# Kernel optimization log

Hardware: AMD Instinct MI355X
Metric: run time of the kernel (lower is better)

The kernel has to match this reference:

```python
import jax, jax.numpy as jnp
import numpy as np

MAX_DISPLACEMENT = 4


def setup_inputs() -> dict:
    key = jax.random.key(0)
    k1, k2 = jax.random.split(key)
    B, C, H, W = 8, 128, 128, 256
    features1 = jax.random.normal(k1, (B, C, H, W), dtype=jnp.float32)
    features2 = jax.random.normal(k2, (B, C, H, W), dtype=jnp.float32)
    return {"features1": features1, "features2": features2}


def _cost_volume(features1, features2, max_displacement):
    B, C, H, W = features1.shape
    d = max_displacement
    # zero-pad features2 spatially by d (uflow compute_cost_volume semantics)
    padded = jnp.pad(features2, ((0, 0), (0, 0), (d, d), (d, d)))
    num_shifts = 2 * d + 1
    costs = []
    for i in range(num_shifts):          # fixed small structural loop: (2d+1)^2 = 81
        for j in range(num_shifts):
            shifted = jax.lax.dynamic_slice(padded, (0, 0, i, j), (B, C, H, W))
            # mean over channel dim of elementwise product
            costs.append(jnp.mean(features1 * shifted, axis=1))
    return jnp.stack(costs, axis=1)  # [B, (2d+1)^2, H, W]


def reference(features1, features2):
    return _cost_volume(features1, features2, MAX_DISPLACEMENT)
```

## Files before the change

kernel.cpp:

```cpp
#include <hip/hip_runtime.h>

#define B_  8
#define C_  128
#define H_  128
#define W_  256
#define HW_ (H_ * W_)
#define TH  8
#define TW  32
#define NPAIR 4
#define F2RS 72
#define F2PT (16 * F2RS)
#define F1RS 36
#define F1PT (8 * F1RS)
#define F1OFF (NPAIR * F2PT)
#define BUFN (F1OFF + NPAIR * F1PT)
#define NTHREADS 576

typedef __fp16 h2 __attribute__((ext_vector_type(2)));

__device__ __forceinline__ float dot2f16(unsigned int a, unsigned int b, float c) {
#if __has_builtin(__builtin_amdgcn_fdot2)
    return __builtin_amdgcn_fdot2(__builtin_bit_cast(h2, a),
                                  __builtin_bit_cast(h2, b), c, false);
#else
    h2 ha = __builtin_bit_cast(h2, a), hb = __builtin_bit_cast(h2, b);
    return c + (float)ha.x * (float)hb.x + (float)ha.y * (float)hb.y;
#endif
}

__device__ __forceinline__ unsigned int pk(float x, float y) {
    h2 r = __builtin_amdgcn_cvt_pkrtz(x, y);
    return __builtin_bit_cast(unsigned int, r);
}

__global__ __launch_bounds__(NTHREADS, 3) void cv_kernel(
    const float* __restrict__ f1g, const float* __restrict__ f2g,
    float* __restrict__ outg) {
    __shared__ __align__(16) unsigned int lds[2][BUFN];

    const int tid = threadIdx.x;
    const int w0 = blockIdx.x * TW;
    const int h0 = blockIdx.y * TH;
    const int b  = blockIdx.z;

    const bool roleA = (tid < 512);
    int offA = 0, ldA = 0;
    float mA = 0.f;
    if (roleA) {
        int pp = tid >> 7, r = (tid >> 3) & 15, u = tid & 7;
        int gh = h0 - 4 + r, gw = w0 - 4 + 4 * u;
        bool valid = (gh >= 0) && (gh < H_) && (gw >= 0) && (gw <= W_ - 4);
        int ghc = min(max(gh, 0), H_ - 1);
        int gwc = min(max(gw, 0), W_ - 4);
        offA = ((b * C_ + 2 * pp) * H_ + ghc) * W_ + gwc;
        ldA  = pp * F2PT + r * F2RS + 4 * u;
        mA   = valid ? 1.f : 0.f;
    }
    const bool roleC = (tid < 384);
    int offC = 0, ldC = 0;
    float mC = 0.f;
    const float* pC = f1g;
    if (tid < 128) {
        int pp = tid >> 5, r = (tid >> 1) & 15, u = 8 + (tid & 1);
        int gh = h0 - 4 + r, gw = w0 - 4 + 4 * u;
        bool valid = (gh >= 0) && (gh < H_) && (gw >= 0) && (gw <= W_ - 4);
        int ghc = min(max(gh, 0), H_ - 1);
        int gwc = min(max(gw, 0), W_ - 4);
        offC = ((b * C_ + 2 * pp) * H_ + ghc) * W_ + gwc;
        pC   = f2g;
        ldC  = pp * F2PT + r * F2RS + 4 * u;
        mC   = valid ? 1.f : 0.f;
    } else if (tid < 384) {
        int t = tid - 128;
        int pp = t >> 6, r = (t >> 3) & 7, u = t & 7;
        offC = ((b * C_ + 2 * pp) * H_ + h0 + r) * W_ + w0 + 4 * u;
        pC   = f1g;
        ldC  = F1OFF + pp * F1PT + r * F1RS + 4 * u;
        mC   = 1.f;
    }

#define LOADST()                                                              \
    do {                                                                      \
        if (roleA) {                                                          \
            aA = *(const float4*)(f2g + offA);                                \
            bA = *(const float4*)(f2g + offA + HW_);                          \
            offA += 8 * HW_;                                                  \
        }                                                                     \
        if (roleC) {                                                          \
            cC = *(const float4*)(pC + offC);                                 \
            dC = *(const float4*)(pC + offC + HW_);                           \
            offC += 8 * HW_;                                                  \
        }                                                                     \
    } while (0)

#define STOREST(bi)                                                           \
    do {                                                                      \
        if (roleA) {                                                          \
            uint4 wv;                                                         \
            wv.x = pk(aA.x * mA, bA.x * mA);                                  \
            wv.y = pk(aA.y * mA, bA.y * mA);                                  \
            wv.z = pk(aA.z * mA, bA.z * mA);                                  \
            wv.w = pk(aA.w * mA, bA.w * mA);                                  \
            *(uint4*)(&lds[bi][ldA]) = wv;                                    \
        }                                                                     \
        if (roleC) {                                                          \
            uint4 w2;                                                         \
            w2.x = pk(cC.x * mC, dC.x * mC);                                  \
            w2.y = pk(cC.y * mC, dC.y * mC);                                  \
            w2.z = pk(cC.z * mC, dC.z * mC);                                  \
            w2.w = pk(cC.w * mC, dC.w * mC);                                  \
            *(uint4*)(&lds[bi][ldC]) = w2;                                    \
        }                                                                     \
    } while (0)

#define BAR()                                                                 \
    do {                                                                      \
        asm volatile("s_waitcnt lgkmcnt(0)" ::: "memory");                    \
        __builtin_amdgcn_s_barrier();                                         \
    } while (0)

    const int di   = tid >> 6;
    const int lane = tid & 63;
    const int hh   = lane >> 3;
    const int sc   = lane & 7;
    const int rd0  = (hh + di) * F2RS + 4 * sc;
    const int rf0  = F1OFF + hh * F1RS + 4 * sc;

    float acc[9][4];
#pragma unroll
    for (int j = 0; j < 9; ++j)
#pragma unroll
        for (int p = 0; p < 4; ++p) acc[j][p] = 0.f;

#define COMPUTE(bi)                                                           \
    do {                                                                      \
        _Pragma("unroll 2")                                                   \
        for (int q = 0; q < NPAIR; ++q) {                                     \
            const unsigned int* bf2 = &lds[bi][q * F2PT];                     \
            const unsigned int* bf1 = &lds[bi][q * F1PT];                     \
            uint4 fa = *(const uint4*)(bf2 + rd0);                            \
            uint4 fb = *(const uint4*)(bf2 + rd0 + 4);                        \
            uint4 fc = *(const uint4*)(bf2 + rd0 + 8);                        \
            uint4 ga = *(const uint4*)(bf1 + rf0);                            \
            unsigned int f2u[12] = {fa.x, fa.y, fa.z, fa.w, fb.x, fb.y,       \
                                    fb.z, fb.w, fc.x, fc.y, fc.z, fc.w};      \
            unsigned int f1u[4]  = {ga.x, ga.y, ga.z, ga.w};                  \
            _Pragma("unroll")                                                 \
            for (int j = 0; j < 9; ++j)                                       \
                _Pragma("unroll")                                             \
                for (int p = 0; p < 4; ++p)                                   \
                    acc[j][p] = dot2f16(f1u[p], f2u[p + j], acc[j][p]);       \
        }                                                                     \
    } while (0)

    float4 aA, bA, cC, dC;

    LOADST();
    STOREST(0);
    BAR();

    for (int st = 0; st < 14; st += 2) {
        LOADST();
        COMPUTE(0);
        STOREST(1);
        BAR();
        LOADST();
        COMPUTE(1);
        STOREST(0);
        BAR();
    }
    LOADST();
    COMPUTE(0);
    STOREST(1);
    BAR();
    COMPUTE(1);

    const float inv = 1.0f / 128.0f;
    int obase = ((b * 81 + di * 9) * H_ + h0 + hh) * W_ + w0 + 4 * sc;
#pragma unroll
    for (int j = 0; j < 9; ++j) {
        float4 o = make_float4(acc[j][0] * inv, acc[j][1] * inv,
                               acc[j][2] * inv, acc[j][3] * inv);
        *(float4*)(outg + obase) = o;
        obase += HW_;
    }
}

extern "C" void kernel_launch(void* const* d_in, const int* in_sizes, int n_in,
                              void* d_out, int out_size, void* d_ws, size_t ws_size,
                              hipStream_t stream) {
    const float* f1 = (const float*)d_in[0];
    const float* f2 = (const float*)d_in[1];
    float* out = (float*)d_out;
    dim3 grid(W_ / TW, H_ / TH, B_);
    cv_kernel<<<grid, NTHREADS, 0, stream>>>(f1, f2, out);
}
```

Baseline: 124.3 us.

## Split displacement rows across three blocks with smaller 192-thread blocks

```diff
diff --git a/kernel.cpp b/kernel.cpp
--- a/kernel.cpp
+++ b/kernel.cpp
@@ -7,14 +7,14 @@
 #define HW_ (H_ * W_)
 #define TH  8
 #define TW  32
-#define NPAIR 4
-#define F2RS 72
-#define F2PT (16 * F2RS)
-#define F1RS 36
-#define F1PT (8 * F1RS)
-#define F1OFF (NPAIR * F2PT)
-#define BUFN (F1OFF + NPAIR * F1PT)
-#define NTHREADS 576
+#define F2R   10
+#define F2RS  48
+#define F2PT  (F2R * F2RS)
+#define F1RS  40
+#define F1PT  (TH * F1RS)
+#define F1OFF (2 * F2PT)
+#define BUFN  (F1OFF + 2 * F1PT)
+#define NTHREADS 192
 
 typedef __fp16 h2 __attribute__((ext_vector_type(2)));
 
@@ -41,75 +41,74 @@
     const int tid = threadIdx.x;
     const int w0 = blockIdx.x * TW;
     const int h0 = blockIdx.y * TH;
-    const int b  = blockIdx.z;
+    const int g  = blockIdx.z % 3;
+    const int b  = blockIdx.z / 3;
+    const int dib = 3 * g;
 
-    const bool roleA = (tid < 512);
-    int offA = 0, ldA = 0;
-    float mA = 0.f;
-    if (roleA) {
-        int pp = tid >> 7, r = (tid >> 3) & 15, u = tid & 7;
-        int gh = h0 - 4 + r, gw = w0 - 4 + 4 * u;
+    int offA, ldA;
+    float mA;
+    {
+        int p  = (tid >= 100);
+        int ul = tid - p * 100;
+        int r  = ul / 10, u = ul - 10 * r;
+        int gh = h0 - 4 + dib + r, gw = w0 - 4 + 4 * u;
         bool valid = (gh >= 0) && (gh < H_) && (gw >= 0) && (gw <= W_ - 4);
         int ghc = min(max(gh, 0), H_ - 1);
         int gwc = min(max(gw, 0), W_ - 4);
-        offA = ((b * C_ + 2 * pp) * H_ + ghc) * W_ + gwc;
-        ldA  = pp * F2PT + r * F2RS + 4 * u;
+        offA = ((b * C_ + 2 * p) * H_ + ghc) * W_ + gwc;
+        ldA  = p * F2PT + r * F2RS + 4 * u;
         mA   = valid ? 1.f : 0.f;
     }
-    const bool roleC = (tid < 384);
+    const bool roleC = (tid < 136);
     int offC = 0, ldC = 0;
     float mC = 0.f;
     const float* pC = f1g;
-    if (tid < 128) {
-        int pp = tid >> 5, r = (tid >> 1) & 15, u = 8 + (tid & 1);
-        int gh = h0 - 4 + r, gw = w0 - 4 + 4 * u;
+    if (tid < 8) {
+        int r = 9, u = 2 + tid;
+        int gh = h0 - 4 + dib + r, gw = w0 - 4 + 4 * u;
         bool valid = (gh >= 0) && (gh < H_) && (gw >= 0) && (gw <= W_ - 4);
         int ghc = min(max(gh, 0), H_ - 1);
         int gwc = min(max(gw, 0), W_ - 4);
-        offC = ((b * C_ + 2 * pp) * H_ + ghc) * W_ + gwc;
+        offC = ((b * C_ + 2) * H_ + ghc) * W_ + gwc;
         pC   = f2g;
-        ldC  = pp * F2PT + r * F2RS + 4 * u;
+        ldC  = F2PT + r * F2RS + 4 * u;
         mC   = valid ? 1.f : 0.f;
-    } else if (tid < 384) {
-        int t = tid - 128;
-        int pp = t >> 6, r = (t >> 3) & 7, u = t & 7;
-        offC = ((b * C_ + 2 * pp) * H_ + h0 + r) * W_ + w0 + 4 * u;
+    } else if (roleC) {
+        int t = tid - 8;
+        int p = t >> 6, r = (t >> 3) & 7, u = t & 7;
+        offC = ((b * C_ + 2 * p) * H_ + h0 + r) * W_ + w0 + 4 * u;
         pC   = f1g;
-        ldC  = F1OFF + pp * F1PT + r * F1RS + 4 * u;
+        ldC  = F1OFF + p * F1PT + r * F1RS + 4 * u;
         mC   = 1.f;
     }
 
 #define LOADST()                                                              \
     do {                                                                      \
-        if (roleA) {                                                          \
-            aA = *(const float4*)(f2g + offA);                                \
-            bA = *(const float4*)(f2g + offA + HW_);                          \
-            offA += 8 * HW_;                                                  \
-        }                                                                     \
+        aA = *(const float4*)(f2g + offA);                                    \
+        bA = *(const float4*)(f2g + offA + HW_);                              \
+        offA += 4 * HW_;                                                      \
         if (roleC) {                                                          \
             cC = *(const float4*)(pC + offC);                                 \
             dC = *(const float4*)(pC + offC + HW_);                           \
-            offC += 8 * HW_;                                                  \
+            offC += 4 * HW_;                                                  \
         }                                                                     \
     } while (0)
 
 #define STOREST(bi)                                                           \
     do {                                                                      \
-        if (roleA) {                                                          \
-            uint4 wv;                                                         \
-            wv.x = pk(aA.x * mA, bA.x * mA);                                  \
-            wv.y = pk(aA.y * mA, bA.y * mA);                                  \
-            wv.z = pk(aA.z * mA, bA.z * mA);                                  \
-            wv.w = pk(aA.w * mA, bA.w * mA);                                  \
-            *(uint4*)(&lds[bi][ldA]) = wv;                                    \
-        }                                                                     \
+        uint4 wv_;                                                            \
+        wv_.x = pk(aA.x * mA, bA.x * mA);                                     \
+        wv_.y = pk(aA.y * mA, bA.y * mA);                                     \
+        wv_.z = pk(aA.z * mA, bA.z * mA);                                     \
+        wv_.w = pk(aA.w * mA, bA.w * mA);                                     \
+        *(uint4*)(&lds[bi][ldA]) = wv_;                                       \
         if (roleC) {                                                          \
-            uint4 w2;                                                         \
-            w2.x = pk(cC.x * mC, dC.x * mC);                                  \
-            w2.y = pk(cC.y * mC, dC.y * mC);                                  \
-            w2.z = pk(cC.z * mC, dC.z * mC);                                  \
-            w2.w = pk(cC.w * mC, dC.w * mC);                                  \
-            *(uint4*)(&lds[bi][ldC]) = w2;                                    \
+            uint4 w2_;                                                        \
+            w2_.x = pk(cC.x * mC, dC.x * mC);                                 \
+            w2_.y = pk(cC.y * mC, dC.y * mC);                                 \
+            w2_.z = pk(cC.z * mC, dC.z * mC);                                 \
+            w2_.w = pk(cC.w * mC, dC.w * mC);                                 \
+            *(uint4*)(&lds[bi][ldC]) = w2_;                                   \
         }                                                                     \
     } while (0)
 
@@ -119,11 +118,11 @@
         __builtin_amdgcn_s_barrier();                                         \
     } while (0)
 
-    const int di   = tid >> 6;
+    const int wv   = tid >> 6;
     const int lane = tid & 63;
     const int hh   = lane >> 3;
     const int sc   = lane & 7;
-    const int rd0  = (hh + di) * F2RS + 4 * sc;
+    const int rd0  = (hh + wv) * F2RS + 4 * sc;
     const int rf0  = F1OFF + hh * F1RS + 4 * sc;
 
     float acc[9][4];
@@ -134,8 +133,8 @@
 
 #define COMPUTE(bi)                                                           \
     do {                                                                      \
-        _Pragma("unroll 2")                                                   \
-        for (int q = 0; q < NPAIR; ++q) {                                     \
+        _Pragma("unroll")                                                     \
+        for (int q = 0; q < 2; ++q) {                                         \
             const unsigned int* bf2 = &lds[bi][q * F2PT];                     \
             const unsigned int* bf1 = &lds[bi][q * F1PT];                     \
             uint4 fa = *(const uint4*)(bf2 + rd0);                            \
@@ -159,7 +158,7 @@
     STOREST(0);
     BAR();
 
-    for (int st = 0; st < 14; st += 2) {
+    for (int st = 0; st < 30; st += 2) {
         LOADST();
         COMPUTE(0);
         STOREST(1);
@@ -176,6 +175,7 @@
     COMPUTE(1);
 
     const float inv = 1.0f / 128.0f;
+    const int di = dib + wv;
     int obase = ((b * 81 + di * 9) * H_ + h0 + hh) * W_ + w0 + 4 * sc;
 #pragma unroll
     for (int j = 0; j < 9; ++j) {
@@ -192,6 +192,6 @@
     const float* f1 = (const float*)d_in[0];
     const float* f2 = (const float*)d_in[1];
     float* out = (float*)d_out;
-    dim3 grid(W_ / TW, H_ / TH, B_);
+    dim3 grid(W_ / TW, H_ / TH, B_ * 3);
     cv_kernel<<<grid, NTHREADS, 0, stream>>>(f1, f2, out);
 }
```

After: 152.7 us. +22.8%, slower.

## Deepen global-load prefetch to two stages and pad f1 LDS row stride

Applied to the files above, without the earlier changes.

```diff
diff --git a/kernel.cpp b/kernel.cpp
--- a/kernel.cpp
+++ b/kernel.cpp
@@ -10,7 +10,7 @@
 #define NPAIR 4
 #define F2RS 72
 #define F2PT (16 * F2RS)
-#define F1RS 36
+#define F1RS 40
 #define F1PT (8 * F1RS)
 #define F1OFF (NPAIR * F2PT)
 #define BUFN (F1OFF + NPAIR * F1PT)
@@ -79,36 +79,36 @@
         mC   = 1.f;
     }
 
-#define LOADST()                                                              \
+#define LOADST(Sa, Sb, Sc, Sd)                                                \
     do {                                                                      \
         if (roleA) {                                                          \
-            aA = *(const float4*)(f2g + offA);                                \
-            bA = *(const float4*)(f2g + offA + HW_);                          \
+            Sa = *(const float4*)(f2g + offA);                                \
+            Sb = *(const float4*)(f2g + offA + HW_);                          \
             offA += 8 * HW_;                                                  \
         }                                                                     \
         if (roleC) {                                                          \
-            cC = *(const float4*)(pC + offC);                                 \
-            dC = *(const float4*)(pC + offC + HW_);                           \
+            Sc = *(const float4*)(pC + offC);                                 \
+            Sd = *(const float4*)(pC + offC + HW_);                           \
             offC += 8 * HW_;                                                  \
         }                                                                     \
     } while (0)
 
-#define STOREST(bi)                                                           \
+#define STOREST(bi, Sa, Sb, Sc, Sd)                                           \
     do {                                                                      \
         if (roleA) {                                                          \
             uint4 wv;                                                         \
-            wv.x = pk(aA.x * mA, bA.x * mA);                                  \
-            wv.y = pk(aA.y * mA, bA.y * mA);                                  \
-            wv.z = pk(aA.z * mA, bA.z * mA);                                  \
-            wv.w = pk(aA.w * mA, bA.w * mA);                                  \
+            wv.x = pk(Sa.x * mA, Sb.x * mA);                                  \
+            wv.y = pk(Sa.y * mA, Sb.y * mA);                                  \
+            wv.z = pk(Sa.z * mA, Sb.z * mA);                                  \
+            wv.w = pk(Sa.w * mA, Sb.w * mA);                                  \
             *(uint4*)(&lds[bi][ldA]) = wv;                                    \
         }                                                                     \
         if (roleC) {                                                          \
             uint4 w2;                                                         \
-            w2.x = pk(cC.x * mC, dC.x * mC);                                  \
-            w2.y = pk(cC.y * mC, dC.y * mC);                                  \
-            w2.z = pk(cC.z * mC, dC.z * mC);                                  \
-            w2.w = pk(cC.w * mC, dC.w * mC);                                  \
+            w2.x = pk(Sc.x * mC, Sd.x * mC);                                  \
+            w2.y = pk(Sc.y * mC, Sd.y * mC);                                  \
+            w2.z = pk(Sc.z * mC, Sd.z * mC);                                  \
+            w2.w = pk(Sc.w * mC, Sd.w * mC);                                  \
             *(uint4*)(&lds[bi][ldC]) = w2;                                    \
         }                                                                     \
     } while (0)
@@ -153,25 +153,25 @@
         }                                                                     \
     } while (0)
 
-    float4 aA, bA, cC, dC;
+    float4 aA, bA, cA, dA, aB, bB, cB, dB;
 
-    LOADST();
-    STOREST(0);
+    LOADST(aA, bA, cA, dA);
+    LOADST(aB, bB, cB, dB);
+    STOREST(0, aA, bA, cA, dA);
     BAR();
 
-    for (int st = 0; st < 14; st += 2) {
-        LOADST();
+    for (int s = 0; s < 14; s += 2) {
+        LOADST(aA, bA, cA, dA);
         COMPUTE(0);
-        STOREST(1);
+        STOREST(1, aB, bB, cB, dB);
         BAR();
-        LOADST();
+        LOADST(aB, bB, cB, dB);
         COMPUTE(1);
-        STOREST(0);
+        STOREST(0, aA, bA, cA, dA);
         BAR();
     }
-    LOADST();
     COMPUTE(0);
-    STOREST(1);
+    STOREST(1, aB, bB, cB, dB);
     BAR();
     COMPUTE(1);
 
```

New measurement: 130.7 us. 5.2% more time.

## Drop ninth wavefront by splitting last displacement row across two waves

Applied to the files above, without the earlier changes.

```diff
diff --git a/kernel.cpp b/kernel.cpp
--- a/kernel.cpp
+++ b/kernel.cpp
@@ -10,11 +10,11 @@
 #define NPAIR 4
 #define F2RS 72
 #define F2PT (16 * F2RS)
-#define F1RS 36
+#define F1RS 40
 #define F1PT (8 * F1RS)
 #define F1OFF (NPAIR * F2PT)
 #define BUFN (F1OFF + NPAIR * F1PT)
-#define NTHREADS 576
+#define NTHREADS 512
 
 typedef __fp16 h2 __attribute__((ext_vector_type(2)));
 
@@ -33,7 +33,7 @@
     return __builtin_bit_cast(unsigned int, r);
 }
 
-__global__ __launch_bounds__(NTHREADS, 3) void cv_kernel(
+__global__ __launch_bounds__(NTHREADS, 4) void cv_kernel(
     const float* __restrict__ f1g, const float* __restrict__ f2g,
     float* __restrict__ outg) {
     __shared__ __align__(16) unsigned int lds[2][BUFN];
@@ -43,10 +43,9 @@
     const int h0 = blockIdx.y * TH;
     const int b  = blockIdx.z;
 
-    const bool roleA = (tid < 512);
-    int offA = 0, ldA = 0;
-    float mA = 0.f;
-    if (roleA) {
+    int offA, ldA;
+    float mA;
+    {
         int pp = tid >> 7, r = (tid >> 3) & 15, u = tid & 7;
         int gh = h0 - 4 + r, gw = w0 - 4 + 4 * u;
         bool valid = (gh >= 0) && (gh < H_) && (gw >= 0) && (gw <= W_ - 4);
@@ -81,11 +80,9 @@
 
 #define LOADST()                                                              \
     do {                                                                      \
-        if (roleA) {                                                          \
-            aA = *(const float4*)(f2g + offA);                                \
-            bA = *(const float4*)(f2g + offA + HW_);                          \
-            offA += 8 * HW_;                                                  \
-        }                                                                     \
+        aA = *(const float4*)(f2g + offA);                                    \
+        bA = *(const float4*)(f2g + offA + HW_);                              \
+        offA += 8 * HW_;                                                      \
         if (roleC) {                                                          \
             cC = *(const float4*)(pC + offC);                                 \
             dC = *(const float4*)(pC + offC + HW_);                           \
@@ -95,14 +92,12 @@
 
 #define STOREST(bi)                                                           \
     do {                                                                      \
-        if (roleA) {                                                          \
-            uint4 wv;                                                         \
-            wv.x = pk(aA.x * mA, bA.x * mA);                                  \
-            wv.y = pk(aA.y * mA, bA.y * mA);                                  \
-            wv.z = pk(aA.z * mA, bA.z * mA);                                  \
-            wv.w = pk(aA.w * mA, bA.w * mA);                                  \
-            *(uint4*)(&lds[bi][ldA]) = wv;                                    \
-        }                                                                     \
+        uint4 wv;                                                             \
+        wv.x = pk(aA.x * mA, bA.x * mA);                                      \
+        wv.y = pk(aA.y * mA, bA.y * mA);                                      \
+        wv.z = pk(aA.z * mA, bA.z * mA);                                      \
+        wv.w = pk(aA.w * mA, bA.w * mA);                                      \
+        *(uint4*)(&lds[bi][ldA]) = wv;                                        \
         if (roleC) {                                                          \
             uint4 w2;                                                         \
             w2.x = pk(cC.x * mC, dC.x * mC);                                  \
@@ -124,13 +119,19 @@
     const int hh   = lane >> 3;
     const int sc   = lane & 7;
     const int rd0  = (hh + di) * F2RS + 4 * sc;
+    const int rd8  = (hh + 8) * F2RS + 4 * sc;
     const int rf0  = F1OFF + hh * F1RS + 4 * sc;
+    const bool sec = (di < 2);
+    const int pxb  = 2 * di;
 
     float acc[9][4];
 #pragma unroll
     for (int j = 0; j < 9; ++j)
 #pragma unroll
         for (int p = 0; p < 4; ++p) acc[j][p] = 0.f;
+    float acc8[9][2];
+#pragma unroll
+    for (int j = 0; j < 9; ++j) { acc8[j][0] = 0.f; acc8[j][1] = 0.f; }
 
 #define COMPUTE(bi)                                                           \
     do {                                                                      \
@@ -138,18 +139,35 @@
         for (int q = 0; q < NPAIR; ++q) {                                     \
             const unsigned int* bf2 = &lds[bi][q * F2PT];                     \
             const unsigned int* bf1 = &lds[bi][q * F1PT];                     \
-            uint4 fa = *(const uint4*)(bf2 + rd0);                            \
-            uint4 fb = *(const uint4*)(bf2 + rd0 + 4);                        \
-            uint4 fc = *(const uint4*)(bf2 + rd0 + 8);                        \
             uint4 ga = *(const uint4*)(bf1 + rf0);                            \
-            unsigned int f2u[12] = {fa.x, fa.y, fa.z, fa.w, fb.x, fb.y,       \
-                                    fb.z, fb.w, fc.x, fc.y, fc.z, fc.w};      \
-            unsigned int f1u[4]  = {ga.x, ga.y, ga.z, ga.w};                  \
-            _Pragma("unroll")                                                 \
-            for (int j = 0; j < 9; ++j)                                       \
+            unsigned int f1u[4] = {ga.x, ga.y, ga.z, ga.w};                   \
+            {                                                                 \
+                uint4 fa = *(const uint4*)(bf2 + rd0);                        \
+                uint4 fb = *(const uint4*)(bf2 + rd0 + 4);                    \
+                uint4 fc = *(const uint4*)(bf2 + rd0 + 8);                    \
+                unsigned int f2u[12] = {fa.x, fa.y, fa.z, fa.w,               \
+                                        fb.x, fb.y, fb.z, fb.w,               \
+                                        fc.x, fc.y, fc.z, fc.w};              \
                 _Pragma("unroll")                                             \
-                for (int p = 0; p < 4; ++p)                                   \
-                    acc[j][p] = dot2f16(f1u[p], f2u[p + j], acc[j][p]);       \
+                for (int j = 0; j < 9; ++j)                                   \
+                    _Pragma("unroll")                                         \
+                    for (int p = 0; p < 4; ++p)                               \
+                        acc[j][p] = dot2f16(f1u[p], f2u[p + j], acc[j][p]);   \
+            }                                                                 \
+            if (sec) {                                                        \
+                uint4 fa = *(const uint4*)(bf2 + rd8);                        \
+                uint4 fb = *(const uint4*)(bf2 + rd8 + 4);                    \
+                uint4 fc = *(const uint4*)(bf2 + rd8 + 8);                    \
+                unsigned int f2u[12] = {fa.x, fa.y, fa.z, fa.w,               \
+                                        fb.x, fb.y, fb.z, fb.w,               \
+                                        fc.x, fc.y, fc.z, fc.w};              \
+                _Pragma("unroll")                                             \
+                for (int j = 0; j < 9; ++j)                                   \
+                    _Pragma("unroll")                                         \
+                    for (int p = 0; p < 2; ++p)                               \
+                        acc8[j][p] = dot2f16(f1u[pxb + p],                    \
+                                             f2u[pxb + p + j], acc8[j][p]);   \
+            }                                                                 \
         }                                                                     \
     } while (0)
 
@@ -184,6 +202,15 @@
         *(float4*)(outg + obase) = o;
         obase += HW_;
     }
+    if (sec) {
+        int o8 = ((b * 81 + 72) * H_ + h0 + hh) * W_ + w0 + 4 * sc + pxb;
+#pragma unroll
+        for (int j = 0; j < 9; ++j) {
+            outg[o8]     = acc8[j][0] * inv;
+            outg[o8 + 1] = acc8[j][1] * inv;
+            o8 += HW_;
+        }
+    }
 }
 
 extern "C" void kernel_launch(void* const* d_in, const int* in_sizes, int n_in,
```

Result: slower. 282.1 us (+127.0%).
